# Optimization experiments

Hardware: AMD Instinct MI355X
Metric: run time of the kernel (lower is better)

## Reference

```python
import jax, jax.numpy as jnp
import numpy as np

B_SZ, T, N, H = 8, 4096, 256, 512  # batch, seq, num_neurons, d_hidden
RMAX, RMIN = 0.99, 0.4


def _glorot_half(k, shape):
    # VarianceScaling(scale=0.5, mode='fan_avg', distribution='uniform')
    fan_avg = (shape[0] + shape[1]) / 2.0
    limit = float(np.sqrt(3.0 * 0.5 / fan_avg))
    return jax.random.uniform(k, shape, jnp.float32, -limit, limit)


def setup_inputs() -> dict:
    key = jax.random.key(0)
    ks = jax.random.split(key, 8)
    x = jax.random.normal(ks[0], (B_SZ, T, N), jnp.float32)
    C_re = _glorot_half(ks[1], (H, N))
    C_im = _glorot_half(ks[2], (H, N))
    B_re = _glorot_half(ks[3], (N, H))
    B_im = _glorot_half(ks[4], (N, H))
    D = jax.random.normal(ks[5], (N,), jnp.float32)
    numin = float(np.log(-np.log(RMAX)))
    numax = float(np.log(-np.log(RMIN)))
    nu = jax.random.uniform(ks[6], (H,), jnp.float32, numin, numax)
    theta = jax.random.uniform(ks[7], (H,), jnp.float32, 0.0, 3.14 / 10)
    lam_abs = jnp.exp(-jnp.exp(nu))  # |lambda| = |exp(-exp(nu) + i*theta)|
    gamma_log = jnp.log(jnp.sqrt(1.0 - lam_abs ** 2))
    return dict(x=x, B_re=B_re, B_im=B_im, C_re=C_re, C_im=C_im,
                D=D, nu=nu, theta=theta, gamma_log=gamma_log)


def _binary_op(qi, qj):
    A_i, b_i = qi
    A_j, b_j = qj
    return (A_j * A_i, A_j * b_i + b_j)


def reference(x, B_re, B_im, C_re, C_im, D, nu, theta, gamma_log):
    u = x  # adapter is identity since n_in == num_neurons
    lam_log = jax.lax.complex(-jnp.exp(nu), theta)            # (H,) log-lambda
    lam = jnp.exp(lam_log)                                     # (H,) diagonal transition
    gamma = jnp.exp(gamma_log).astype(jnp.complex64)           # (H,)
    Bm = jax.lax.complex(B_re, B_im)                           # (N,H)
    Cm = jax.lax.complex(C_re, C_im)                           # (H,N)
    u_c = u.astype(jnp.complex64)
    bu = gamma * (u_c @ Bm)                                    # (B,T,H) complex64
    A = jnp.broadcast_to(lam, (1, u.shape[1], lam.shape[0]))   # (1,T,H), broadcasts in op
    _, xs = jax.lax.associative_scan(_binary_op, (A, bu), axis=1)  # (B,T,H)
    y = jnp.real(xs @ Cm) + D * u                              # (B,T,N) float32
    return y
```

## Files before the change

### kernel.cpp

```cpp
#include <hip/hip_runtime.h>

#define B_SZ 8
#define T_LEN 4096
#define N_DIM 256
#define H_DIM 512
#define NC 32
#define CL 128
#define ROWS (B_SZ * T_LEN)

#define BM 128
#define BN 128
#define BKg 32

typedef __attribute__((ext_vector_type(4))) float f32x4;
typedef __attribute__((ext_vector_type(8))) short bf16x8;

static __device__ __forceinline__ unsigned short f2bf(float f) {
    unsigned int u = __float_as_uint(f);
    unsigned int r = (u + 0x7FFFu + ((u >> 16) & 1u)) >> 16;
    return (unsigned short)r;
}
static __device__ __forceinline__ float bf2f(unsigned short s) {
    return __uint_as_float(((unsigned int)s) << 16);
}

static __device__ __forceinline__ void lam_of(const float* __restrict__ nu,
                                              const float* __restrict__ theta,
                                              int h, float& lre, float& lim) {
    float r = __expf(-__expf(nu[h]));
    float th = theta[h];
    lre = r * __cosf(th);
    lim = r * __sinf(th);
}

__global__ __launch_bounds__(256) void conv_x(const float4* __restrict__ x, ushort4* __restrict__ xb) {
    int id = blockIdx.x * 256 + threadIdx.x;
    float4 v = x[id];
    ushort4 o;
    o.x = f2bf(v.x); o.y = f2bf(v.y); o.z = f2bf(v.z); o.w = f2bf(v.w);
    xb[id] = o;
}

__global__ __launch_bounds__(256) void conv_Bt(const float* __restrict__ Bre,
                                               const float* __restrict__ Bim,
                                               unsigned short* __restrict__ BT1) {
    int id = blockIdx.x * 256 + threadIdx.x;
    int k = id >> 9, h = id & 511;
    BT1[(long)(2 * h) * 256 + k]     = f2bf(Bre[id]);
    BT1[(long)(2 * h + 1) * 256 + k] = f2bf(Bim[id]);
}

__global__ __launch_bounds__(256) void conv_Ct(const float* __restrict__ Cre,
                                               const float* __restrict__ Cim,
                                               unsigned short* __restrict__ CT) {
    int id = blockIdx.x * 256 + threadIdx.x;
    int h = id >> 8, nn = id & 255;
    CT[(long)nn * 1024 + 2 * h]     = f2bf(Cre[id]);
    CT[(long)nn * 1024 + 2 * h + 1] = f2bf(-Cim[id]);
}

template <int MODE>
__global__ __launch_bounds__(256) void gemm_mfma(const unsigned short* __restrict__ A,
                                                 const unsigned short* __restrict__ Bt,
                                                 int M, int N, int K,
                                                 const float* __restrict__ e0,
                                                 const float* __restrict__ e1,
                                                 const unsigned short* __restrict__ e1b,
                                                 void* __restrict__ out) {
    __shared__ unsigned short As[3][BM * BKg];
    __shared__ unsigned short Bs[3][BN * BKg];
    const int tid = threadIdx.x;
    const int lane = tid & 63;
    const int wave = tid >> 6;
    const int wr = wave >> 1, wc = wave & 1;

    const int nwg = (int)gridDim.x;
    const int cpx = nwg >> 3;
    const int bid = (int)blockIdx.x;
    const int tile = (bid & 7) * cpx + (bid >> 3);

    const int nTilesN = N / BN;
    const long tileM = (long)(tile / nTilesN) * BM;
    const long tileN = (long)(tile % nTilesN) * BN;

    const int rsub = lane >> 2;
    const int sg = 8 * ((lane & 3) ^ ((lane >> 3) & 3));
    const unsigned short* Abase = A + tileM * (long)K + sg;
    const unsigned short* Bbase = Bt + tileN * (long)K + sg;

    auto stage = [&](int buf, int k0) {
#pragma unroll
        for (int cc = 0; cc < 2; ++cc) {
            const int c = wave + cc * 4;
            const int row = c * 16 + rsub;
            const unsigned short* ga = Abase + (long)row * K + k0;
            __builtin_amdgcn_global_load_lds((const __attribute__((address_space(1))) unsigned int*)ga,
                                             (__attribute__((address_space(3))) unsigned int*)(As[buf] + c * 512),
                                             16, 0, 0);
            const unsigned short* gb = Bbase + (long)row * K + k0;
            __builtin_amdgcn_global_load_lds((const __attribute__((address_space(1))) unsigned int*)gb,
                                             (__attribute__((address_space(3))) unsigned int*)(Bs[buf] + c * 512),
                                             16, 0, 0);
        }
    };

    const int rdA = 16 * ((lane >> 4) ^ ((lane >> 1) & 3));

    f32x4 acc[4][4] = {};
    const int nt = K / BKg;

    stage(0, 0);
    stage(1, BKg);

    int cur = 0, pf = 2;
    for (int t = 0; t < nt; ++t) {
        if (t + 2 < nt) {
            stage(pf, (t + 2) * BKg);
            asm volatile("s_waitcnt vmcnt(8)" ::: "memory");
        } else if (t + 1 < nt) {
            asm volatile("s_waitcnt vmcnt(4)" ::: "memory");
        } else {
            asm volatile("s_waitcnt vmcnt(0)" ::: "memory");
        }
        __builtin_amdgcn_s_barrier();
        asm volatile("" ::: "memory");

        bf16x8 af[4], bfr[4];
#pragma unroll
        for (int m = 0; m < 4; ++m) {
            const int row = wr * 64 + m * 16 + (lane & 15);
            af[m] = *(const bf16x8*)((const char*)As[cur] + row * 64 + rdA);
        }
#pragma unroll
        for (int n = 0; n < 4; ++n) {
            const int row = wc * 64 + n * 16 + (lane & 15);
            bfr[n] = *(const bf16x8*)((const char*)Bs[cur] + row * 64 + rdA);
        }
#pragma unroll
        for (int m = 0; m < 4; ++m)
#pragma unroll
            for (int n = 0; n < 4; ++n)
                acc[m][n] = __builtin_amdgcn_mfma_f32_16x16x32_bf16(bfr[n], af[m], acc[m][n], 0, 0, 0);

        asm volatile("" ::: "memory");
        __builtin_amdgcn_s_barrier();
        asm volatile("" ::: "memory");

        cur = (cur == 2) ? 0 : cur + 1;
        pf = (pf == 2) ? 0 : pf + 1;
    }

    const int fr = lane & 15;
    const int fs = lane >> 4;
    if constexpr (MODE == 0) {
        unsigned short* o = (unsigned short*)out;
#pragma unroll
        for (int n = 0; n < 4; ++n) {
            const int col0 = (int)tileN + wc * 64 + n * 16 + fs * 4;
            const int h0 = col0 >> 1;
            const float g0 = __expf(e0[h0]);
            const float g1 = __expf(e0[h0 + 1]);
#pragma unroll
            for (int m = 0; m < 4; ++m) {
                const long grow = tileM + wr * 64 + m * 16 + fr;
                ushort4 pk;
                pk.x = f2bf(acc[m][n][0] * g0);
                pk.y = f2bf(acc[m][n][1] * g0);
                pk.z = f2bf(acc[m][n][2] * g1);
                pk.w = f2bf(acc[m][n][3] * g1);
                *(ushort4*)(o + grow * N + col0) = pk;
            }
        }
    } else {
        float* o = (float*)out;
#pragma unroll
        for (int n = 0; n < 4; ++n) {
            const int col0 = (int)tileN + wc * 64 + n * 16 + fs * 4;
            const float4 dv = *(const float4*)(e0 + col0);
#pragma unroll
            for (int m = 0; m < 4; ++m) {
                const long grow = tileM + wr * 64 + m * 16 + fr;
                const long idx = grow * N + col0;
                float u0, u1, u2, u3;
                if (e1b) {
                    ushort4 ub = *(const ushort4*)(e1b + idx);
                    u0 = bf2f(ub.x); u1 = bf2f(ub.y); u2 = bf2f(ub.z); u3 = bf2f(ub.w);
                } else {
                    float4 uf = *(const float4*)(e1 + idx);
                    u0 = uf.x; u1 = uf.y; u2 = uf.z; u3 = uf.w;
                }
                float4 st;
                st.x = acc[m][n][0] + dv.x * u0;
                st.y = acc[m][n][1] + dv.y * u1;
                st.z = acc[m][n][2] + dv.z * u2;
                st.w = acc[m][n][3] + dv.w * u3;
                *(float4*)(o + idx) = st;
            }
        }
    }
}


__global__ __launch_bounds__(256) void k2s_sums(const ushort4* __restrict__ xs4,
                                                float4* __restrict__ sums,
                                                const float* __restrict__ nu,
                                                const float* __restrict__ theta) {
    const int gid = blockIdx.x * 256 + threadIdx.x;
    const int hp = gid & 255;
    const int c = (gid >> 8) & (NC - 1);
    const int b = gid >> 13;
    float lre0, lim0, lre1, lim1;
    lam_of(nu, theta, 2 * hp, lre0, lim0);
    lam_of(nu, theta, 2 * hp + 1, lre1, lim1);
    long base = ((long)b * T_LEN + (long)c * CL) * 256 + hp;
    float a0r = 0.f, a0i = 0.f, a1r = 0.f, a1i = 0.f;
#pragma unroll 4
    for (int i = 0; i < CL; ++i) {
        ushort4 v = xs4[base + (long)i * 256];
        float u0r = bf2f(v.x), u0i = bf2f(v.y), u1r = bf2f(v.z), u1i = bf2f(v.w);
        float n0r = fmaf(lre0, a0r, fmaf(-lim0, a0i, u0r));
        float n0i = fmaf(lre0, a0i, fmaf(lim0, a0r, u0i));
        float n1r = fmaf(lre1, a1r, fmaf(-lim1, a1i, u1r));
        float n1i = fmaf(lre1, a1i, fmaf(lim1, a1r, u1i));
        a0r = n0r; a0i = n0i; a1r = n1r; a1i = n1i;
    }
    sums[((long)b * NC + c) * 256 + hp] = make_float4(a0r, a0i, a1r, a1i);
}

__global__ __launch_bounds__(256) void k2b_carry(const float4* __restrict__ sums,
                                                 float4* __restrict__ carry,
                                                 const float* __restrict__ nu,
                                                 const float* __restrict__ theta) {
    const int gid = blockIdx.x * 256 + threadIdx.x;
    const int hp = gid & 255;
    const int b = gid >> 8;
    float lre0, lim0, lre1, lim1;
    lam_of(nu, theta, 2 * hp, lre0, lim0);
    lam_of(nu, theta, 2 * hp + 1, lre1, lim1);
    float p0r = lre0, p0i = lim0, p1r = lre1, p1i = lim1;
#pragma unroll
    for (int i = 0; i < 7; ++i) {
        float t0 = p0r * p0r - p0i * p0i; p0i = 2.f * p0r * p0i; p0r = t0;
        float t1 = p1r * p1r - p1i * p1i; p1i = 2.f * p1r * p1i; p1r = t1;
    }
    float c0r = 0.f, c0i = 0.f, c1r = 0.f, c1i = 0.f;
    for (int c = 0; c < NC; ++c) {
        long idx = ((long)b * NC + c) * 256 + hp;
        carry[idx] = make_float4(c0r, c0i, c1r, c1i);
        float4 s = sums[idx];
        float t0 = fmaf(p0r, c0r, fmaf(-p0i, c0i, s.x));
        c0i = fmaf(p0r, c0i, fmaf(p0i, c0r, s.y));
        c0r = t0;
        float t1 = fmaf(p1r, c1r, fmaf(-p1i, c1i, s.z));
        c1i = fmaf(p1r, c1i, fmaf(p1i, c1r, s.w));
        c1r = t1;
    }
}

__global__ __launch_bounds__(256) void k2ac_scan(ushort4* __restrict__ xs4,
                                                 const float4* __restrict__ carry,
                                                 const float* __restrict__ nu,
                                                 const float* __restrict__ theta) {
    const int gid = blockIdx.x * 256 + threadIdx.x;
    const int hp = gid & 255;
    const int c = (gid >> 8) & (NC - 1);
    const int b = gid >> 13;
    float lre0, lim0, lre1, lim1;
    lam_of(nu, theta, 2 * hp, lre0, lim0);
    lam_of(nu, theta, 2 * hp + 1, lre1, lim1);
    float4 cr = carry[((long)b * NC + c) * 256 + hp];
    float a0r = cr.x, a0i = cr.y, a1r = cr.z, a1i = cr.w;
    long base = ((long)b * T_LEN + (long)c * CL) * 256 + hp;
#pragma unroll 4
    for (int i = 0; i < CL; ++i) {
        ushort4 v = xs4[base + (long)i * 256];
        float u0r = bf2f(v.x), u0i = bf2f(v.y), u1r = bf2f(v.z), u1i = bf2f(v.w);
        float n0r = fmaf(lre0, a0r, fmaf(-lim0, a0i, u0r));
        float n0i = fmaf(lre0, a0i, fmaf(lim0, a0r, u0i));
        float n1r = fmaf(lre1, a1r, fmaf(-lim1, a1i, u1r));
        float n1i = fmaf(lre1, a1i, fmaf(lim1, a1r, u1i));
        a0r = n0r; a0i = n0i; a1r = n1r; a1i = n1i;
        ushort4 o;
        o.x = f2bf(a0r); o.y = f2bf(a0i); o.z = f2bf(a1r); o.w = f2bf(a1i);
        xs4[base + (long)i * 256] = o;
    }
}

extern "C" void kernel_launch(void* const* d_in, const int* in_sizes, int n_in,
                              void* d_out, int out_size, void* d_ws, size_t ws_size,
                              hipStream_t stream) {
    const float* x         = (const float*)d_in[0];
    const float* Bre       = (const float*)d_in[1];
    const float* Bim       = (const float*)d_in[2];
    const float* Cre       = (const float*)d_in[3];
    const float* Cim       = (const float*)d_in[4];
    const float* Dv        = (const float*)d_in[5];
    const float* nu        = (const float*)d_in[6];
    const float* theta     = (const float*)d_in[7];
    const float* gamma_log = (const float*)d_in[8];
    float* y = (float*)d_out;

    const size_t XS_BYTES  = (size_t)ROWS * H_DIM * 4;
    const size_t REG_BYTES = 2u * 1024 * 1024;
    const size_t XB_BYTES  = (size_t)ROWS * N_DIM * 2;
    unsigned short* xs_us = (unsigned short*)d_ws;
    ushort4* xs4   = (ushort4*)d_ws;
    char* regionA  = (char*)d_ws + XS_BYTES;
    char* regionB  = regionA + REG_BYTES;
    unsigned short* BT1 = (unsigned short*)regionA;
    float4*  sums  = (float4*)regionA;
    unsigned short* CT  = (unsigned short*)regionA;
    float4*  carry = (float4*)regionB;

    const bool xb_in_ws = ws_size >= XS_BYTES + 2 * REG_BYTES + XB_BYTES;
    unsigned short* xb = xb_in_ws ? (unsigned short*)(regionB + REG_BYTES)
                                  : (unsigned short*)d_out;

    conv_x<<<ROWS * N_DIM / 4 / 256, 256, 0, stream>>>((const float4*)x, (ushort4*)xb);
    conv_Bt<<<(N_DIM * H_DIM) / 256, 256, 0, stream>>>(Bre, Bim, BT1);

    gemm_mfma<0><<<(ROWS / BM) * (1024 / BN), 256, 0, stream>>>(xb, BT1, ROWS, 1024, 256,
                                                                gamma_log, nullptr, nullptr, xs_us);
    k2s_sums<<<(B_SZ * NC * 256) / 256, 256, 0, stream>>>(xs4, sums, nu, theta);
    k2b_carry<<<(B_SZ * 256) / 256, 256, 0, stream>>>(sums, carry, nu, theta);
    k2ac_scan<<<(B_SZ * NC * 256) / 256, 256, 0, stream>>>(xs4, carry, nu, theta);

    conv_Ct<<<(H_DIM * N_DIM) / 256, 256, 0, stream>>>(Cre, Cim, CT);

    gemm_mfma<1><<<(ROWS / BM) * (256 / BN), 256, 0, stream>>>(xs_us, CT, ROWS, 256, 1024,
                                                               Dv, x, xb_in_ws ? xb : nullptr, y);
}
```

Measured before the change: 129.3 us.

## Fuse chunk-sum reduction of the scan into first GEMM epilogue

Computes the per-chunk weighted sums (lambda^(127-t) * bu) directly from the fp32 accumulators in the B-projection GEMM epilogue. It reduces them with wave shuffles and shared memory and writes them to the sums buffer. This removes the separate k2s_sums kernel, which re-read the whole bf16 xs tensor sequentially. The epilogue gains transcendental and shuffle work, and the sums now come from unrounded fp32 values instead of bf16, which slightly changes numerics. The sums buffer moves to regionB so it does not overlap CT/BT1.

```diff
diff --git a/kernel.cpp b/kernel.cpp
--- a/kernel.cpp
+++ b/kernel.cpp
@@ -33,6 +33,33 @@
     lim = r * __sinf(th);
 }
 
+static __device__ __forceinline__ void csum4(const float* __restrict__ nu,
+                                             const float* __restrict__ theta,
+                                             int h, int pb,
+                                             const float* ur, const float* ui,
+                                             float& outr, float& outi) {
+    const float e  = __expf(nu[h]);
+    const float th = theta[h];
+    const float p3 = (float)(pb - 48);
+    const float r3 = __expf(-p3 * e);
+    float w_r = r3 * __cosf(p3 * th);
+    float w_i = r3 * __sinf(p3 * th);
+    const float r16 = __expf(-16.f * e);
+    const float l_r = r16 * __cosf(16.f * th);
+    const float l_i = r16 * __sinf(16.f * th);
+    float sr = w_r * ur[3] - w_i * ui[3];
+    float si = w_r * ui[3] + w_i * ur[3];
+#pragma unroll
+    for (int m = 2; m >= 0; --m) {
+        const float nwr = w_r * l_r - w_i * l_i;
+        const float nwi = w_r * l_i + w_i * l_r;
+        w_r = nwr; w_i = nwi;
+        sr += w_r * ur[m] - w_i * ui[m];
+        si += w_r * ui[m] + w_i * ur[m];
+    }
+    outr = sr; outi = si;
+}
+
 __global__ __launch_bounds__(256) void conv_x(const float4* __restrict__ x, ushort4* __restrict__ xb) {
     int id = blockIdx.x * 256 + threadIdx.x;
     float4 v = x[id];
@@ -66,9 +93,12 @@
                                                  const float* __restrict__ e0,
                                                  const float* __restrict__ e1,
                                                  const unsigned short* __restrict__ e1b,
+                                                 const float* __restrict__ nu,
+                                                 const float* __restrict__ theta,
+                                                 float4* __restrict__ sums,
                                                  void* __restrict__ out) {
-    __shared__ unsigned short As[3][BM * BKg];
-    __shared__ unsigned short Bs[3][BN * BKg];
+    __shared__ __align__(16) unsigned short As[3][BM * BKg];
+    __shared__ __align__(16) unsigned short Bs[3][BN * BKg];
     const int tid = threadIdx.x;
     const int lane = tid & 63;
     const int wave = tid >> 6;
@@ -154,22 +184,52 @@
     const int fs = lane >> 4;
     if constexpr (MODE == 0) {
         unsigned short* o = (unsigned short*)out;
+        float s_r0[4], s_i0[4], s_r1[4], s_i1[4];
+        const int pb = 127 - wr * 64 - fr;
 #pragma unroll
         for (int n = 0; n < 4; ++n) {
             const int col0 = (int)tileN + wc * 64 + n * 16 + fs * 4;
             const int h0 = col0 >> 1;
             const float g0 = __expf(e0[h0]);
             const float g1 = __expf(e0[h0 + 1]);
+            float ur0[4], ui0[4], ur1[4], ui1[4];
 #pragma unroll
             for (int m = 0; m < 4; ++m) {
                 const long grow = tileM + wr * 64 + m * 16 + fr;
+                const float v0 = acc[m][n][0] * g0;
+                const float v1 = acc[m][n][1] * g0;
+                const float v2 = acc[m][n][2] * g1;
+                const float v3 = acc[m][n][3] * g1;
                 ushort4 pk;
-                pk.x = f2bf(acc[m][n][0] * g0);
-                pk.y = f2bf(acc[m][n][1] * g0);
-                pk.z = f2bf(acc[m][n][2] * g1);
-                pk.w = f2bf(acc[m][n][3] * g1);
+                pk.x = f2bf(v0); pk.y = f2bf(v1); pk.z = f2bf(v2); pk.w = f2bf(v3);
                 *(ushort4*)(o + grow * N + col0) = pk;
+                ur0[m] = v0; ui0[m] = v1; ur1[m] = v2; ui1[m] = v3;
             }
+            csum4(nu, theta, h0,     pb, ur0, ui0, s_r0[n], s_i0[n]);
+            csum4(nu, theta, h0 + 1, pb, ur1, ui1, s_r1[n], s_i1[n]);
+        }
+#pragma unroll
+        for (int n = 0; n < 4; ++n) {
+#pragma unroll
+            for (int st = 1; st < 16; st <<= 1) {
+                s_r0[n] += __shfl_xor(s_r0[n], st);
+                s_i0[n] += __shfl_xor(s_i0[n], st);
+                s_r1[n] += __shfl_xor(s_r1[n], st);
+                s_i1[n] += __shfl_xor(s_i1[n], st);
+            }
+        }
+        __syncthreads();
+        float4* red = (float4*)As;
+        if (fr == 0) {
+#pragma unroll
+            for (int n = 0; n < 4; ++n)
+                red[wr * 32 + wc * 16 + n * 4 + fs] = make_float4(s_r0[n], s_i0[n], s_r1[n], s_i1[n]);
+        }
+        __syncthreads();
+        if (tid < 32) {
+            float4 a = red[tid], b2 = red[32 + tid];
+            sums[(long)(tileM >> 7) * 256 + (tileN >> 2) + tid] =
+                make_float4(a.x + b2.x, a.y + b2.y, a.z + b2.z, a.w + b2.w);
         }
     } else {
         float* o = (float*)out;
@@ -201,32 +261,6 @@
 }
 
 
-__global__ __launch_bounds__(256) void k2s_sums(const ushort4* __restrict__ xs4,
-                                                float4* __restrict__ sums,
-                                                const float* __restrict__ nu,
-                                                const float* __restrict__ theta) {
-    const int gid = blockIdx.x * 256 + threadIdx.x;
-    const int hp = gid & 255;
-    const int c = (gid >> 8) & (NC - 1);
-    const int b = gid >> 13;
-    float lre0, lim0, lre1, lim1;
-    lam_of(nu, theta, 2 * hp, lre0, lim0);
-    lam_of(nu, theta, 2 * hp + 1, lre1, lim1);
-    long base = ((long)b * T_LEN + (long)c * CL) * 256 + hp;
-    float a0r = 0.f, a0i = 0.f, a1r = 0.f, a1i = 0.f;
-#pragma unroll 4
-    for (int i = 0; i < CL; ++i) {
-        ushort4 v = xs4[base + (long)i * 256];
-        float u0r = bf2f(v.x), u0i = bf2f(v.y), u1r = bf2f(v.z), u1i = bf2f(v.w);
-        float n0r = fmaf(lre0, a0r, fmaf(-lim0, a0i, u0r));
-        float n0i = fmaf(lre0, a0i, fmaf(lim0, a0r, u0i));
-        float n1r = fmaf(lre1, a1r, fmaf(-lim1, a1i, u1r));
-        float n1i = fmaf(lre1, a1i, fmaf(lim1, a1r, u1i));
-        a0r = n0r; a0i = n0i; a1r = n1r; a1i = n1i;
-    }
-    sums[((long)b * NC + c) * 256 + hp] = make_float4(a0r, a0i, a1r, a1i);
-}
-
 __global__ __launch_bounds__(256) void k2b_carry(const float4* __restrict__ sums,
                                                  float4* __restrict__ carry,
                                                  const float* __restrict__ nu,
@@ -244,6 +278,7 @@
         float t1 = p1r * p1r - p1i * p1i; p1i = 2.f * p1r * p1i; p1r = t1;
     }
     float c0r = 0.f, c0i = 0.f, c1r = 0.f, c1i = 0.f;
+#pragma unroll
     for (int c = 0; c < NC; ++c) {
         long idx = ((long)b * NC + c) * 256 + hp;
         carry[idx] = make_float4(c0r, c0i, c1r, c1i);
@@ -308,9 +343,9 @@
     char* regionA  = (char*)d_ws + XS_BYTES;
     char* regionB  = regionA + REG_BYTES;
     unsigned short* BT1 = (unsigned short*)regionA;
-    float4*  sums  = (float4*)regionA;
     unsigned short* CT  = (unsigned short*)regionA;
     float4*  carry = (float4*)regionB;
+    float4*  sums  = (float4*)(regionB + 1024 * 1024);
 
     const bool xb_in_ws = ws_size >= XS_BYTES + 2 * REG_BYTES + XB_BYTES;
     unsigned short* xb = xb_in_ws ? (unsigned short*)(regionB + REG_BYTES)
@@ -319,14 +354,14 @@
     conv_x<<<ROWS * N_DIM / 4 / 256, 256, 0, stream>>>((const float4*)x, (ushort4*)xb);
     conv_Bt<<<(N_DIM * H_DIM) / 256, 256, 0, stream>>>(Bre, Bim, BT1);
 
-    gemm_mfma<0><<<(ROWS / BM) * (1024 / BN), 256, 0, stream>>>(xb, BT1, ROWS, 1024, 256,
-                                                                gamma_log, nullptr, nullptr, xs_us);
-    k2s_sums<<<(B_SZ * NC * 256) / 256, 256, 0, stream>>>(xs4, sums, nu, theta);
+    gemm_mfma<0><<<(ROWS / BM) * (1024 / BN), 256, 0, stream>>>(
+        xb, BT1, ROWS, 1024, 256, gamma_log, nullptr, nullptr, nu, theta, sums, xs_us);
+
     k2b_carry<<<(B_SZ * 256) / 256, 256, 0, stream>>>(sums, carry, nu, theta);
     k2ac_scan<<<(B_SZ * NC * 256) / 256, 256, 0, stream>>>(xs4, carry, nu, theta);
 
     conv_Ct<<<(H_DIM * N_DIM) / 256, 256, 0, stream>>>(Cre, Cim, CT);
 
-    gemm_mfma<1><<<(ROWS / BM) * (256 / BN), 256, 0, stream>>>(xs_us, CT, ROWS, 256, 1024,
-                                                               Dv, x, xb_in_ws ? xb : nullptr, y);
-}
+    gemm_mfma<1><<<(ROWS / BM) * (256 / BN), 256, 0, stream>>>(
+        xs_us, CT, ROWS, 256, 1024, Dv, x, xb_in_ws ? xb : nullptr, nullptr, nullptr, nullptr, y);
+}
```

Result: faster. 122.0 us, median of 2 (-5.6%).
